# Performance work log

Measured on AMD Instinct MI355X. Metric: run time of the kernel, lower is better.

The kernel has to match this reference:

```python
import jax, jax.numpy as jnp
import numpy as np

TARGET_SIZE = 48
START_TAG = 46
END_TAG = 47
MINIMUM = -10000.0
BATCH = 256
SEQ = 2048


def setup_inputs() -> dict:
    key = jax.random.key(0)
    k1, k2, k3 = jax.random.split(key, 3)
    features = jax.random.normal(k1, (BATCH, SEQ, TARGET_SIZE), dtype=jnp.float32)
    transitions = jax.random.normal(k2, (TARGET_SIZE, TARGET_SIZE), dtype=jnp.float32)
    # CRF constraints: nothing transitions *from* after START row semantics in this repo:
    # transitions[START_TAG, :] = min (can't transition into START... per repo convention)
    transitions = transitions.at[START_TAG, :].set(MINIMUM)
    transitions = transitions.at[:, END_TAG].set(MINIMUM)
    seq_len = jax.random.randint(k3, (BATCH,), 1, SEQ + 1, dtype=jnp.int32)
    return {"features": features, "transitions": transitions, "seq_len": seq_len}


def reference(features, transitions, seq_len):
    """CRF forward algorithm (log partition) per sample.

    features: [B, S, T] emission scores
    transitions: [T, T], transitions[next, prev]
    seq_len: [B] true lengths; alpha is read at step seq_len[b]
    returns: [B] log partition score
    """
    B, S, T = features.shape
    init_alpha = jnp.full((B, T), MINIMUM, dtype=features.dtype).at[:, START_TAG].set(0.0)

    def step(alpha, emit):  # alpha [B,T] over prev tags, emit [B,T] over next tags
        # tag_var[b, next, prev] = emit[b, next] + transitions[next, prev] + alpha[b, prev]
        tag_var = emit[:, :, None] + transitions[None, :, :] + alpha[:, None, :]
        new_alpha = jax.nn.logsumexp(tag_var, axis=2)  # [B, T]
        return new_alpha, new_alpha

    _, alphas = jax.lax.scan(step, init_alpha, jnp.swapaxes(features, 0, 1))  # [S, B, T]
    all_alpha = jnp.concatenate([init_alpha[None], alphas], axis=0)  # [S+1, B, T]
    idx = seq_len.astype(jnp.int32)
    alpha_at_len = all_alpha[idx, jnp.arange(B)]  # [B, T]
    terminal = alpha_at_len + transitions[END_TAG][None, :]
    return jax.nn.logsumexp(terminal, axis=1)  # [B]
```

## Files before the change

### kernel.cpp

```cpp
#include <hip/hip_runtime.h>

#define BATCH 256
#define SEQ 2048
#define NT 48
#define START_TAG 46
#define END_TAG 47
#define LN2f  0.6931471805599453f

#define TAF16 0
#define TBF   4608
#define TCUM  13824
#define TSC   16384
#define TW    131072

typedef float v2f __attribute__((ext_vector_type(2)));
typedef float v4f __attribute__((ext_vector_type(4)));
typedef short s16x4 __attribute__((ext_vector_type(4)));
typedef unsigned int u32;
typedef u32 u32x2 __attribute__((ext_vector_type(2)));
typedef u32 u32x4 __attribute__((ext_vector_type(4)));

__device__ __forceinline__ u32 pkbf(float a, float b) {
    u32 r;
    asm("v_cvt_pk_bf16_f32 %0, %1, %2" : "=v"(r) : "v"(a), "v"(b));
    return r;
}
__device__ __forceinline__ float bflo(u32 w) { return __builtin_bit_cast(float, w << 16); }
__device__ __forceinline__ float bfhi(u32 w) { return __builtin_bit_cast(float, w & 0xffff0000u); }

__device__ __forceinline__ float rfl(float x) {
    return __builtin_bit_cast(float,
        __builtin_amdgcn_readfirstlane(__builtin_bit_cast(int, x)));
}

__device__ __forceinline__ v4f mfma16_z(s16x4 a, s16x4 b, v4f z) {
    v4f d;
    asm volatile("v_mfma_f32_16x16x16_bf16 %0, %2, %3, %1"
                 : "=&v"(d) : "v"(z), "v"(a), "v"(b));
    return d;
}
__device__ __forceinline__ void mfma16_acc(v4f& acc, s16x4 a, s16x4 b) {
    asm volatile("v_mfma_f32_16x16x16_bf16 %0, %1, %2, %0"
                 : "+v"(acc) : "v"(a), "v"(b));
}

__global__ void __launch_bounds__(64)
crf_setup(const float* __restrict__ trans, const int* __restrict__ seqlen,
          void* ws) {
    __shared__ float el[NT * NT];
    const int lane = threadIdx.x, ln = lane & 15, g = lane >> 4;
    #pragma unroll
    for (int m = 0; m < 36; ++m) {
        int idx = lane + 64 * m;
        el[idx] = __expf(trans[idx]);
    }
    u32x2* AF = (u32x2*)((char*)ws + TAF16);
    v4f*   BF = (v4f*)((char*)ws + TBF);
    #pragma unroll
    for (int I = 0; I < 3; ++I)
        #pragma unroll
        for (int K = 0; K < 3; ++K) {
            const v4f ev = *(const v4f*)&el[(I * 16 + ln) * NT + K * 16 + g * 4];
            AF[(I * 3 + K) * 64 + lane] = (u32x2){pkbf(ev.x, ev.y), pkbf(ev.z, ev.w)};
        }
    #pragma unroll
    for (int K = 0; K < 3; ++K)
        #pragma unroll
        for (int J = 0; J < 3; ++J) {
            v4f v;
            #pragma unroll
            for (int i = 0; i < 4; ++i)
                v[i] = el[(K * 16 + g * 4 + i) * NT + J * 16 + ln];
            BF[(K * 3 + J) * 64 + lane] = v;
        }
    if (lane == 0) {
        int* cum = (int*)((char*)ws + TCUM);
        int acc = 0;
        for (int b = 0; b < BATCH; ++b) {
            cum[b] = acc;
            int L = seqlen[b];
            if (L < 1) L = 1;
            if (L > SEQ) L = SEQ;
            acc += (L + 31) >> 5;
        }
        cum[BATCH] = acc;
    }
}

__global__ void __launch_bounds__(256, 4)
crf_phase1c(const float* __restrict__ feat, const int* __restrict__ seqlen,
            void* __restrict__ ws) {
    const int wid = threadIdx.x >> 6;
    const int widx = blockIdx.x * 4 + wid;
    const int* cum = (const int*)((const char*)ws + TCUM);
    if (widx >= cum[BATCH]) return;

    int lo = 0, hi = BATCH;
    #pragma unroll
    for (int it = 0; it < 8; ++it) {
        int mid = (lo + hi) >> 1;
        if (cum[mid] <= widx) lo = mid; else hi = mid;
    }
    const int b = lo;
    const int c = widx - cum[b];
    const int t0 = c * 32;
    const int L = seqlen[b];
    int n = L - t0;
    if (n > 32) n = 32;

    const int lane = threadIdx.x & 63, ln = lane & 15, g = lane >> 4;

    __shared__ v4f flv[4][32 * 12 + 16];
    v4f* fl = flv[wid];

    s16x4 aw[3][3];
    {
        const u32x2* AF = (const u32x2*)((const char*)ws + TAF16);
        #pragma unroll
        for (int I = 0; I < 3; ++I)
            #pragma unroll
            for (int K = 0; K < 3; ++K)
                aw[I][K] = __builtin_bit_cast(s16x4, AF[(I * 3 + K) * 64 + lane]);
    }

    {
        const v4f* fg = (const v4f*)(feat + ((size_t)b * SEQ + t0) * NT);
        #pragma unroll
        for (int m = 0; m < 6; ++m) {
            v4f v = fg[m * 64 + lane];
            v4f e;
            #pragma unroll
            for (int i = 0; i < 4; ++i) e[i] = __expf(v[i]);
            fl[m * 64 + lane] = e;
        }
    }

    s16x4 mw[3][3];
    {
        const v4f* BF = (const v4f*)((const char*)ws + TBF);
        v4f em[3];
        #pragma unroll
        for (int K = 0; K < 3; ++K) em[K] = fl[K * 4 + g];
        #pragma unroll
        for (int K = 0; K < 3; ++K)
            #pragma unroll
            for (int J = 0; J < 3; ++J) {
                v4f sc = BF[(K * 3 + J) * 64 + lane] * em[K];
                mw[K][J] = __builtin_bit_cast(s16x4,
                    (u32x2){pkbf(sc.x, sc.y), pkbf(sc.z, sc.w)});
            }
    }

    float Lc = 0.f, lg = 0.f, s = 1.f;
    const v4f kz = {0.f, 0.f, 0.f, 0.f};

    for (int t = 1; t < n; ++t) {
        v4f em[3];
        #pragma unroll
        for (int K = 0; K < 3; ++K) em[K] = fl[t * 12 + K * 4 + g];

        v4f acc[3][3];
        #pragma unroll
        for (int I = 0; I < 3; ++I)
            #pragma unroll
            for (int J = 0; J < 3; ++J)
                acc[I][J] = mfma16_z(aw[I][0], mw[0][J], kz);
        #pragma unroll
        for (int I = 0; I < 3; ++I)
            #pragma unroll
            for (int J = 0; J < 3; ++J)
                mfma16_acc(acc[I][J], aw[I][1], mw[1][J]);
        #pragma unroll
        for (int I = 0; I < 3; ++I)
            #pragma unroll
            for (int J = 0; J < 3; ++J)
                mfma16_acc(acc[I][J], aw[I][2], mw[2][J]);
        asm volatile("s_nop 7\n\ts_nop 7");
        __builtin_amdgcn_sched_barrier(0);

        const float gn = rfl(acc[0][0].x);
        Lc += lg;
        #pragma unroll
        for (int K = 0; K < 3; ++K) {
            v4f sp = em[K] * s;
            #pragma unroll
            for (int J = 0; J < 3; ++J) {
                v4f sc = acc[K][J] * sp;
                mw[K][J] = __builtin_bit_cast(s16x4,
                    (u32x2){pkbf(sc.x, sc.y), pkbf(sc.z, sc.w)});
            }
        }
        lg = __log2f(gn);
        s  = __builtin_amdgcn_rcpf(gn);
    }

    char* wb = (char*)ws + TW + ((size_t)(b * 64 + c)) * 4608;
    #pragma unroll
    for (int K = 0; K < 3; ++K)
        #pragma unroll
        for (int J = 0; J < 3; ++J) {
            u32x2 w = __builtin_bit_cast(u32x2, mw[K][J]);
            *(u32*)(wb + 2 * ((J * 16 + ln) * NT + K * 16 + g * 4))     = w.x;
            *(u32*)(wb + 2 * ((J * 16 + ln) * NT + K * 16 + g * 4 + 2)) = w.y;
        }
    if (lane == 0)
        ((float*)((char*)ws + TSC))[b * 64 + c] = Lc;
}

__global__ void __launch_bounds__(64)
crf_phase2(const float* __restrict__ trans, const int* __restrict__ seqlen,
           const void* __restrict__ ws, float* __restrict__ out) {
    const int b = blockIdx.x;
    const int lane = threadIdx.x;
    const int j = (lane < NT) ? lane : (lane - 16);
    __shared__ v4f hs4[12];
    float* hs = (float*)hs4;

    const int L = seqlen[b];
    const int nb = (L + 31) / 32;
    const float* sc = (const float*)((const char*)ws + TSC) + b * 64;
    const char* wbase = (const char*)ws + TW + (size_t)b * 64 * 4608;

    float q = __expf(trans[END_TAG * NT + j]);
    float D = 0.f;

    u32x4 buf[6];
    {
        const u32x4* wr = (const u32x4*)(wbase + (size_t)(nb - 1) * 4608 + j * 96);
        #pragma unroll
        for (int m = 0; m < 6; ++m) buf[m] = wr[m];
    }

    for (int c = nb - 1; c >= 0; --c) {
        u32x4 cur[6];
        #pragma unroll
        for (int m = 0; m < 6; ++m) cur[m] = buf[m];
        if (c > 0) {
            const u32x4* wr = (const u32x4*)(wbase + (size_t)(c - 1) * 4608 + j * 96);
            #pragma unroll
            for (int m = 0; m < 6; ++m) buf[m] = wr[m];
        }

        if (lane < NT) hs[lane] = q;
        v4f hq[12];
        #pragma unroll
        for (int k = 0; k < 12; ++k) hq[k] = hs4[k];
        const float h0 = hq[0][0];

        v2f a = {0.f, 0.f};
        #pragma unroll
        for (int m = 0; m < 6; ++m) {
            #pragma unroll
            for (int p = 0; p < 4; ++p) {
                const int i = 2 * (4 * m + p);
                u32 wv = cur[m][p];
                v2f wp;
                wp.x = bflo(wv);
                wp.y = bfhi(wv);
                v2f up = { hq[i >> 2][i & 3], hq[i >> 2][(i & 3) + 1] };
                a += wp * up;
            }
        }
        const float dot = a.x + a.y;
        q = dot * __builtin_amdgcn_rcpf(h0);
        D += __log2f(h0) + sc[c];
    }
    if (lane < NT) hs[lane] = q;
    if (lane == 0)
        out[b] = LN2f * (D + __log2f(hs[START_TAG]));
}

__global__ void __launch_bounds__(64)
crf_scalar(const float* __restrict__ features, const float* __restrict__ transitions,
           const int* __restrict__ seq_len, float* __restrict__ out) {
    const int b = blockIdx.x;
    const int lane = threadIdx.x;
    const int j = (lane < NT) ? lane : (lane - 16);
    __shared__ v4f hs4[NT / 4];
    float* hs = (float*)hs4;

    v2f E2[NT / 2];
    {
        const v4f* trow = (const v4f*)(transitions + j * NT);
        #pragma unroll
        for (int k = 0; k < NT / 4; ++k) {
            v4f tv = trow[k];
            E2[2 * k].x = __expf(tv.x); E2[2 * k].y = __expf(tv.y);
            E2[2 * k + 1].x = __expf(tv.z); E2[2 * k + 1].y = __expf(tv.w);
        }
    }
    const float Eend = __expf(transitions[END_TAG * NT + j]);
    const int L = seq_len[b];
    const float* fbase = features + ((size_t)b * SEQ) * NT + j;

    float q = E2[START_TAG / 2].x * __expf(fbase[0]);
    float Clog2 = 0.0f;
    if (lane < NT) hs[lane] = q;

    float fb[8];
    #pragma unroll
    for (int u = 0; u < 8; ++u) {
        int tp = 1 + u;
        fb[u] = fbase[(size_t)(tp < SEQ ? tp : 0) * NT];
    }

    auto STEP = [&](float femit) {
        v4f hq[NT / 4];
        #pragma unroll
        for (int k = 0; k < NT / 4; ++k) hq[k] = hs4[k];
        float h0 = hq[0].x;
        float r = __builtin_amdgcn_rcpf(h0);
        float e = __expf(femit);
        float re = r * e;
        v2f a0 = {0.f, 0.f}, a1 = {0.f, 0.f};
        #pragma unroll
        for (int k = 0; k < NT / 4; ++k) {
            v2f lo = { hq[k].x, hq[k].y };
            v2f hi = { hq[k].z, hq[k].w };
            a0 += E2[2 * k] * lo;
            a1 += E2[2 * k + 1] * hi;
        }
        float d = (a0.x + a1.x) + (a0.y + a1.y);
        q = d * re;
        Clog2 += __log2f(h0);
        if (lane < NT) hs[lane] = q;
    };

    int t = 1;
    while (t + 8 <= L) {
        #pragma unroll
        for (int u = 0; u < 8; ++u) {
            STEP(fb[u]);
            int tp = t + u + 8;
            fb[u] = fbase[(size_t)(tp < SEQ ? tp : 0) * NT];
        }
        t += 8;
    }
    #pragma unroll
    for (int u = 0; u < 8; ++u)
        if (t + u < L) STEP(fb[u]);

    float term = (lane < NT) ? q * Eend : 0.0f;
    #pragma unroll
    for (int m = 32; m >= 1; m >>= 1) term += __shfl_xor(term, m, 64);
    if (lane == 0) out[b] = LN2f * (Clog2 + __log2f(term));
}

extern "C" void kernel_launch(void* const* d_in, const int* in_sizes, int n_in,
                              void* d_out, int out_size, void* d_ws, size_t ws_size,
                              hipStream_t stream) {
    const float* features    = (const float*)d_in[0];
    const float* transitions = (const float*)d_in[1];
    const int*   seqlen      = (const int*)d_in[2];
    float* out = (float*)d_out;

    const size_t need = (size_t)TW + (size_t)BATCH * 64 * 4608;
    if (ws_size >= need) {
        crf_setup<<<1, 64, 0, stream>>>(transitions, seqlen, d_ws);
        crf_phase1c<<<4096, 256, 0, stream>>>(features, seqlen, d_ws);
        crf_phase2<<<BATCH, 64, 0, stream>>>(transitions, seqlen, d_ws, out);
    } else {
        crf_scalar<<<BATCH, 64, 0, stream>>>(features, transitions, seqlen, out);
    }
}
```

Baseline: 130.5 us.

## Split chunk-matrix chain into forward and backward halves across two waves

Phase 2 serially chained per-chunk 48x48 transfer matrices from the end back to the start in one wave. It now uses two waves per sample. One wave propagates backward from the end-tag vector over the upper half of the chunks, the other propagates forward from the start-tag vector over the lower half, and the two results are combined with a dot product. Phase 1 stores lower-half chunk matrices transposed so the forward wave can read them row-wise, which adds scattered 16-bit stores. This roughly halves the serial dependency chain per sample.

Measured after the change: 121.0 us. -7.3%, faster.

```diff
diff --git a/kernel.cpp b/kernel.cpp
--- a/kernel.cpp
+++ b/kernel.cpp
@@ -17,6 +17,7 @@
 typedef float v4f __attribute__((ext_vector_type(4)));
 typedef short s16x4 __attribute__((ext_vector_type(4)));
 typedef unsigned int u32;
+typedef unsigned short u16;
 typedef u32 u32x2 __attribute__((ext_vector_type(2)));
 typedef u32 u32x4 __attribute__((ext_vector_type(4)));
 
@@ -104,13 +105,17 @@
     const int b = lo;
     const int c = widx - cum[b];
     const int t0 = c * 32;
-    const int L = seqlen[b];
-    int n = L - t0;
+    int Lraw = seqlen[b];
+    if (Lraw < 1) Lraw = 1;
+    if (Lraw > SEQ) Lraw = SEQ;
+    const int nbS = (Lraw + 31) >> 5;
+    const int half = nbS >> 1;
+    int n = Lraw - t0;
     if (n > 32) n = 32;
 
     const int lane = threadIdx.x & 63, ln = lane & 15, g = lane >> 4;
 
-    __shared__ v4f flv[4][32 * 12 + 16];
+    __shared__ v4f flv[4][32 * 12];
     v4f* fl = flv[wid];
 
     s16x4 aw[3][3];
@@ -195,79 +200,120 @@
     }
 
     char* wb = (char*)ws + TW + ((size_t)(b * 64 + c)) * 4608;
-    #pragma unroll
-    for (int K = 0; K < 3; ++K)
-        #pragma unroll
-        for (int J = 0; J < 3; ++J) {
-            u32x2 w = __builtin_bit_cast(u32x2, mw[K][J]);
-            *(u32*)(wb + 2 * ((J * 16 + ln) * NT + K * 16 + g * 4))     = w.x;
-            *(u32*)(wb + 2 * ((J * 16 + ln) * NT + K * 16 + g * 4 + 2)) = w.y;
-        }
+    if (c >= half) {
+        #pragma unroll
+        for (int K = 0; K < 3; ++K)
+            #pragma unroll
+            for (int J = 0; J < 3; ++J) {
+                u32x2 w = __builtin_bit_cast(u32x2, mw[K][J]);
+                *(u32*)(wb + 2 * ((J * 16 + ln) * NT + K * 16 + g * 4))     = w.x;
+                *(u32*)(wb + 2 * ((J * 16 + ln) * NT + K * 16 + g * 4 + 2)) = w.y;
+            }
+    } else {
+        u16* mb = (u16*)wb;
+        #pragma unroll
+        for (int K = 0; K < 3; ++K)
+            #pragma unroll
+            for (int J = 0; J < 3; ++J) {
+                u32x2 w = __builtin_bit_cast(u32x2, mw[K][J]);
+                const int r0 = K * 16 + g * 4, col = J * 16 + ln;
+                mb[(r0 + 0) * NT + col] = (u16)(w.x & 0xffff);
+                mb[(r0 + 1) * NT + col] = (u16)(w.x >> 16);
+                mb[(r0 + 2) * NT + col] = (u16)(w.y & 0xffff);
+                mb[(r0 + 3) * NT + col] = (u16)(w.y >> 16);
+            }
+    }
     if (lane == 0)
         ((float*)((char*)ws + TSC))[b * 64 + c] = Lc;
 }
 
-__global__ void __launch_bounds__(64)
-crf_phase2(const float* __restrict__ trans, const int* __restrict__ seqlen,
-           const void* __restrict__ ws, float* __restrict__ out) {
+__global__ void __launch_bounds__(128)
+crf_phase2s(const float* __restrict__ trans, const int* __restrict__ seqlen,
+            const void* __restrict__ ws, float* __restrict__ out) {
     const int b = blockIdx.x;
-    const int lane = threadIdx.x;
+    const int wave = threadIdx.x >> 6;
+    const int lane = threadIdx.x & 63;
     const int j = (lane < NT) ? lane : (lane - 16);
-    __shared__ v4f hs4[12];
-    float* hs = (float*)hs4;
-
-    const int L = seqlen[b];
-    const int nb = (L + 31) / 32;
+
+    __shared__ v4f hsv[2][12];
+    __shared__ float sres[2][NT];
+    __shared__ float sD[2];
+    float* hs = (float*)hsv[wave];
+
+    int L = seqlen[b];
+    if (L < 1) L = 1;
+    if (L > SEQ) L = SEQ;
+    const int nb = (L + 31) >> 5;
+    const int half = nb >> 1;
     const float* sc = (const float*)((const char*)ws + TSC) + b * 64;
     const char* wbase = (const char*)ws + TW + (size_t)b * 64 * 4608;
 
-    float q = __expf(trans[END_TAG * NT + j]);
+    const int c0   = wave ? 0 : (nb - 1);
+    const int cend = wave ? (half - 1) : half;
+    const int cstep = wave ? 1 : -1;
+    const int nhops = wave ? half : (nb - half);
+
+    float q = wave ? ((j == START_TAG) ? 1.f : 0.f)
+                   : __expf(trans[END_TAG * NT + j]);
     float D = 0.f;
 
-    u32x4 buf[6];
-    {
-        const u32x4* wr = (const u32x4*)(wbase + (size_t)(nb - 1) * 4608 + j * 96);
-        #pragma unroll
-        for (int m = 0; m < 6; ++m) buf[m] = wr[m];
-    }
-
-    for (int c = nb - 1; c >= 0; --c) {
-        u32x4 cur[6];
-        #pragma unroll
-        for (int m = 0; m < 6; ++m) cur[m] = buf[m];
-        if (c > 0) {
-            const u32x4* wr = (const u32x4*)(wbase + (size_t)(c - 1) * 4608 + j * 96);
+    if (nhops > 0) {
+        u32x4 buf[6];
+        {
+            const u32x4* wr = (const u32x4*)(wbase + (size_t)c0 * 4608 + j * 96);
             #pragma unroll
             for (int m = 0; m < 6; ++m) buf[m] = wr[m];
         }
-
-        if (lane < NT) hs[lane] = q;
-        v4f hq[12];
-        #pragma unroll
-        for (int k = 0; k < 12; ++k) hq[k] = hs4[k];
-        const float h0 = hq[0][0];
-
-        v2f a = {0.f, 0.f};
-        #pragma unroll
-        for (int m = 0; m < 6; ++m) {
-            #pragma unroll
-            for (int p = 0; p < 4; ++p) {
-                const int i = 2 * (4 * m + p);
-                u32 wv = cur[m][p];
-                v2f wp;
-                wp.x = bflo(wv);
-                wp.y = bfhi(wv);
-                v2f up = { hq[i >> 2][i & 3], hq[i >> 2][(i & 3) + 1] };
-                a += wp * up;
-            }
-        }
-        const float dot = a.x + a.y;
-        q = dot * __builtin_amdgcn_rcpf(h0);
-        D += __log2f(h0) + sc[c];
-    }
-    if (lane < NT) hs[lane] = q;
-    if (lane == 0)
-        out[b] = LN2f * (D + __log2f(hs[START_TAG]));
+        for (int hh = 0; hh < nhops; ++hh) {
+            const int c = c0 + hh * cstep;
+            u32x4 cur[6];
+            #pragma unroll
+            for (int m = 0; m < 6; ++m) cur[m] = buf[m];
+            if (hh + 1 < nhops) {
+                const u32x4* wr =
+                    (const u32x4*)(wbase + (size_t)(c + cstep) * 4608 + j * 96);
+                #pragma unroll
+                for (int m = 0; m < 6; ++m) buf[m] = wr[m];
+            }
+
+            if (lane < NT) hs[lane] = q;
+            v4f hq[12];
+            #pragma unroll
+            for (int k = 0; k < 12; ++k) hq[k] = hsv[wave][k];
+            const float h0 = hq[0][0];
+
+            v2f a = {0.f, 0.f};
+            #pragma unroll
+            for (int m = 0; m < 6; ++m) {
+                #pragma unroll
+                for (int p = 0; p < 4; ++p) {
+                    const int i = 2 * (4 * m + p);
+                    u32 wv = cur[m][p];
+                    v2f wp;
+                    wp.x = bflo(wv);
+                    wp.y = bfhi(wv);
+                    v2f up = { hq[i >> 2][i & 3], hq[i >> 2][(i & 3) + 1] };
+                    a += wp * up;
+                }
+            }
+            const float dot = a.x + a.y;
+            const bool ok = (h0 > 0.f);
+            q = ok ? dot * __builtin_amdgcn_rcpf(h0) : dot;
+            D += (ok ? __log2f(h0) : 0.f) + sc[c];
+        }
+    }
+
+    if (lane < NT) sres[wave][j] = q;
+    if (lane == 0) sD[wave] = D;
+    __syncthreads();
+
+    if (wave == 0) {
+        float term = (lane < NT) ? sres[0][lane] * sres[1][lane] : 0.f;
+        #pragma unroll
+        for (int m = 32; m >= 1; m >>= 1) term += __shfl_xor(term, m, 64);
+        if (lane == 0)
+            out[b] = LN2f * (sD[0] + sD[1] + __log2f(term));
+    }
 }
 
 __global__ void __launch_bounds__(64)
@@ -358,7 +404,7 @@
     if (ws_size >= need) {
         crf_setup<<<1, 64, 0, stream>>>(transitions, seqlen, d_ws);
         crf_phase1c<<<4096, 256, 0, stream>>>(features, seqlen, d_ws);
-        crf_phase2<<<BATCH, 64, 0, stream>>>(transitions, seqlen, d_ws, out);
+        crf_phase2s<<<BATCH, 128, 0, stream>>>(transitions, seqlen, d_ws, out);
     } else {
         crf_scalar<<<BATCH, 64, 0, stream>>>(features, transitions, seqlen, out);
     }
```
